# Optimization experiments

Hardware: AMD Instinct MI355X
Metric: run time of the kernel (lower is better)

The kernel has to match this reference:

```python
import jax, jax.numpy as jnp
import numpy as np

EPS = 1e-5

def _layernorm(x, gamma, beta):
    mu = jnp.mean(x, axis=-1, keepdims=True)
    var = jnp.var(x, axis=-1, keepdims=True)
    return (x - mu) * jax.lax.rsqrt(var + EPS) * gamma + beta

def setup_inputs() -> dict:
    key = jax.random.key(0)
    ks = jax.random.split(key, 6)
    bs, t, dim = 4, 2048, 1024
    x = jax.random.normal(ks[0], (bs, t, dim), dtype=jnp.float32)
    # shared LayerNorm params (same module applied twice in forward)
    ln_gamma = jnp.ones((dim,), dtype=jnp.float32)
    ln_beta = jnp.zeros((dim,), dtype=jnp.float32)
    # Linear params, stored as (in, out)
    w1 = jax.random.normal(ks[1], (dim, 2 * dim), dtype=jnp.float32) / np.sqrt(dim)
    b1 = jax.random.normal(ks[2], (2 * dim,), dtype=jnp.float32) * 0.01
    w2 = jax.random.normal(ks[3], (2 * dim, dim), dtype=jnp.float32) / np.sqrt(2 * dim)
    b2 = jax.random.normal(ks[4], (dim,), dtype=jnp.float32) * 0.01
    return {"x": x, "ln_gamma": ln_gamma, "ln_beta": ln_beta,
            "w1": w1, "b1": b1, "w2": w2, "b2": b2}

def reference(x, ln_gamma, ln_beta, w1, b1, w2, b2):
    # x: [bs, t, f]
    y = _layernorm(x, ln_gamma, ln_beta)
    y = jax.nn.gelu(jnp.einsum('btf,fh->bth', y, w1) + b1, approximate=False)
    y = jnp.einsum('bth,hf->btf', y, w2) + b2
    # attention-like quadratic mix (no softmax): (x @ x^T) @ y
    scores = jnp.einsum('btf,bsf->bts', x, x)          # [bs, t, t]
    y = jnp.einsum('bts,bsf->btf', scores, y)
    y = x + y
    y = _layernorm(y, ln_gamma, ln_beta)
    return y
```

## Files before the change

### kernel.cpp

```cpp
#include <hip/hip_runtime.h>
#include <hip/hip_fp16.h>

typedef _Float16 f16;
typedef _Float16 f16x8 __attribute__((ext_vector_type(8)));
typedef _Float16 f16x4 __attribute__((ext_vector_type(4)));
typedef float f32x4 __attribute__((ext_vector_type(4)));

#define LN_EPS 1e-5f

__device__ __forceinline__ float erf_fast(float x) {
    const float ax = __builtin_fabsf(x);
    const float t = 1.0f / (1.0f + 0.3275911f * ax);
    const float y = t * (0.254829592f +
                    t * (-0.284496736f +
                    t * (1.421413741f +
                    t * (-1.453152027f +
                    t * 1.061405429f))));
    const float r = 1.0f - y * __expf(-ax * ax);
    return __builtin_copysignf(r, x);
}

__device__ __forceinline__ float gelu_exact(float v) {
    return 0.5f * v * (1.0f + erf_fast(v * 0.70710678118654752440f));
}

__device__ __forceinline__ void gload_lds16(const f16* g, f16* l) {
    __builtin_amdgcn_global_load_lds(
        (const __attribute__((address_space(1))) unsigned int*)(g),
        (__attribute__((address_space(3))) unsigned int*)(l),
        16, 0, 0);
}

__global__ __launch_bounds__(256)
void ln_cast_kernel(const float* __restrict__ x,
                    const float* __restrict__ gamma,
                    const float* __restrict__ beta,
                    f16* __restrict__ y_h,
                    f16* __restrict__ x_h) {
    const int row = blockIdx.x;
    const int t = threadIdx.x;
    const size_t base = (size_t)row * 1024;
    float4 v = ((const float4*)(x + base))[t];
    float s  = v.x + v.y + v.z + v.w;
    float s2 = v.x*v.x + v.y*v.y + v.z*v.z + v.w*v.w;
    #pragma unroll
    for (int off = 32; off > 0; off >>= 1) {
        s  += __shfl_down(s, off, 64);
        s2 += __shfl_down(s2, off, 64);
    }
    __shared__ float ls[4], ls2[4];
    const int wid = t >> 6;
    if ((t & 63) == 0) { ls[wid] = s; ls2[wid] = s2; }
    __syncthreads();
    if (t == 0) {
        ls[0]  = ls[0] + ls[1] + ls[2] + ls[3];
        ls2[0] = ls2[0] + ls2[1] + ls2[2] + ls2[3];
    }
    __syncthreads();
    const float mu   = ls[0] * (1.0f / 1024.0f);
    const float var  = ls2[0] * (1.0f / 1024.0f) - mu * mu;
    const float rstd = rsqrtf(var + LN_EPS);
    const float4 g  = ((const float4*)gamma)[t];
    const float4 bt = ((const float4*)beta)[t];
    f16x4 yo, xo;
    yo[0] = (f16)((v.x - mu) * rstd * g.x + bt.x);
    yo[1] = (f16)((v.y - mu) * rstd * g.y + bt.y);
    yo[2] = (f16)((v.z - mu) * rstd * g.z + bt.z);
    yo[3] = (f16)((v.w - mu) * rstd * g.w + bt.w);
    xo[0] = (f16)v.x; xo[1] = (f16)v.y; xo[2] = (f16)v.z; xo[3] = (f16)v.w;
    *(f16x4*)(y_h + base + t * 4) = yo;
    *(f16x4*)(x_h + base + t * 4) = xo;
}

__global__ __launch_bounds__(256)
void ln_final_kernel(const f16* __restrict__ pre,
                     const float* __restrict__ gamma,
                     const float* __restrict__ beta,
                     float* __restrict__ out) {
    const int row = blockIdx.x;
    const int t = threadIdx.x;
    const size_t base = (size_t)row * 1024;
    const f16x4 vh = *(const f16x4*)(pre + base + t * 4);
    float4 v;
    v.x = (float)vh[0]; v.y = (float)vh[1]; v.z = (float)vh[2]; v.w = (float)vh[3];
    float s  = v.x + v.y + v.z + v.w;
    float s2 = v.x*v.x + v.y*v.y + v.z*v.z + v.w*v.w;
    #pragma unroll
    for (int off = 32; off > 0; off >>= 1) {
        s  += __shfl_down(s, off, 64);
        s2 += __shfl_down(s2, off, 64);
    }
    __shared__ float ls[4], ls2[4];
    const int wid = t >> 6;
    if ((t & 63) == 0) { ls[wid] = s; ls2[wid] = s2; }
    __syncthreads();
    if (t == 0) {
        ls[0]  = ls[0] + ls[1] + ls[2] + ls[3];
        ls2[0] = ls2[0] + ls2[1] + ls2[2] + ls2[3];
    }
    __syncthreads();
    const float mu   = ls[0] * (1.0f / 1024.0f);
    const float var  = ls2[0] * (1.0f / 1024.0f) - mu * mu;
    const float rstd = rsqrtf(var + LN_EPS);
    const float4 g  = ((const float4*)gamma)[t];
    const float4 bt = ((const float4*)beta)[t];
    float4 o;
    o.x = (v.x - mu) * rstd * g.x + bt.x;
    o.y = (v.y - mu) * rstd * g.y + bt.y;
    o.z = (v.z - mu) * rstd * g.z + bt.z;
    o.w = (v.w - mu) * rstd * g.w + bt.w;
    ((float4*)(out + base))[t] = o;
}

__global__ __launch_bounds__(256)
void transpose_cast_kernel(const float* __restrict__ src,
                           f16* __restrict__ dst, int R, int C) {
    __shared__ float tile[32][33];
    const int c0 = blockIdx.x * 32, r0 = blockIdx.y * 32;
    const int tx = threadIdx.x & 31, ty = threadIdx.x >> 5;
    #pragma unroll
    for (int i = 0; i < 4; ++i) {
        const int r = ty + i * 8;
        tile[r][tx] = src[(size_t)(r0 + r) * C + c0 + tx];
    }
    __syncthreads();
    #pragma unroll
    for (int i = 0; i < 4; ++i) {
        const int r = ty + i * 8;
        dst[(size_t)(c0 + r) * R + r0 + tx] = (f16)tile[tx][r];
    }
}

__global__ __launch_bounds__(256)
void transpose_f16_kernel(const f16* __restrict__ src,
                          f16* __restrict__ dst, int R, int C) {
    __shared__ f16 tile[32][33];
    const size_t zb = (size_t)blockIdx.z * R * C;
    src += zb; dst += zb;
    const int c0 = blockIdx.x * 32, r0 = blockIdx.y * 32;
    const int tx = threadIdx.x & 31, ty = threadIdx.x >> 5;
    #pragma unroll
    for (int i = 0; i < 4; ++i) {
        const int r = ty + i * 8;
        tile[r][tx] = src[(size_t)(r0 + r) * C + c0 + tx];
    }
    __syncthreads();
    #pragma unroll
    for (int i = 0; i < 4; ++i) {
        const int r = ty + i * 8;
        dst[(size_t)(c0 + r) * R + r0 + tx] = tile[tx][r];
    }
}

template <int EPI>
__global__ __launch_bounds__(512, 2)
void gemm256x128_nt_kernel(const f16* __restrict__ A, const f16* __restrict__ Bt,
                           const float* __restrict__ bias,
                           const float* __restrict__ xadd,
                           f16* __restrict__ outH,
                           int M, int N, int K,
                           long long batchA, long long batchB, long long batchC) {
    __shared__ __attribute__((aligned(16))) f16 sA[3][256 * 64];
    __shared__ __attribute__((aligned(16))) f16 sB[3][128 * 64];

    const int z = blockIdx.z;
    A  += (size_t)z * batchA;
    Bt += (size_t)z * batchB;

    const int m0 = blockIdx.x * 256;
    const int n0 = blockIdx.y * 128;
    const int t = threadIdx.x;
    const int l = t & 63;
    const int wid = t >> 6;
    const int wr = wid >> 1;
    const int wc = wid & 1;
    const int rl = l & 15;
    const int g  = l >> 4;
    const int nk = K >> 6;

    const int rowS = t >> 3;
    const int kbS  = ((t & 7) ^ (rowS & 7)) * 8;
    const f16* pA = A  + (size_t)(m0 + rowS) * K + kbS;
    const f16* pB = Bt + (size_t)(n0 + rowS) * K + kbS;
    const int ldsS = wid * 512;

    const int rA = wr * 64 + rl;
    const int rB = wc * 64 + rl;
    const int swk0 = ((g)     ^ (rl & 7)) * 8;
    const int swk1 = ((4 + g) ^ (rl & 7)) * 8;

    f32x4 acc[4][4] = {};

    auto mf = [&](f32x4 c, f16x8 af, f16x8 bf) {
        if constexpr (EPI != 1)
            return __builtin_amdgcn_mfma_f32_16x16x32_f16(bf, af, c, 0, 0, 0);
        else
            return __builtin_amdgcn_mfma_f32_16x16x32_f16(af, bf, c, 0, 0, 0);
    };

    auto stgA = [&](f16* dst, int u, int kc) {
        gload_lds16(pA + (size_t)u * 64 * K + kc * 64, dst + u * 4096 + ldsS);
    };
    auto stgB = [&](f16* dst, int u, int kc) {
        gload_lds16(pB + (size_t)u * 64 * K + kc * 64, dst + u * 4096 + ldsS);
    };

    const int t1 = (nk > 1) ? 1 : 0;
    #pragma unroll
    for (int u = 0; u < 4; ++u) stgA(sA[0], u, 0);
    #pragma unroll
    for (int u = 0; u < 2; ++u) stgB(sB[0], u, 0);
    #pragma unroll
    for (int u = 0; u < 4; ++u) stgA(sA[1], u, t1);
    #pragma unroll
    for (int u = 0; u < 2; ++u) stgB(sB[1], u, t1);

    f16 *curA = sA[0], *nxtA = sA[1], *farA = sA[2];
    f16 *curB = sB[0], *nxtB = sB[1], *farB = sB[2];

    f16x8 a[4][2], b[4][2];

    for (int kt = 0; kt < nk; ++kt) {
        asm volatile("s_waitcnt vmcnt(6)" ::: "memory");
        __builtin_amdgcn_s_barrier();

        const int kt2 = (kt + 2 < nk) ? kt + 2 : nk - 1;

        #pragma unroll
        for (int fm = 0; fm < 2; ++fm) {
            a[fm][0] = *(const f16x8*)(curA + (rA + fm * 16) * 64 + swk0);
            a[fm][1] = *(const f16x8*)(curA + (rA + fm * 16) * 64 + swk1);
        }
        #pragma unroll
        for (int fn = 0; fn < 2; ++fn) {
            b[fn][0] = *(const f16x8*)(curB + (rB + fn * 16) * 64 + swk0);
            b[fn][1] = *(const f16x8*)(curB + (rB + fn * 16) * 64 + swk1);
        }
        stgA(farA, 0, kt2);
        stgA(farA, 1, kt2);
        asm volatile("s_waitcnt lgkmcnt(0)" ::: "memory");
        __builtin_amdgcn_sched_barrier(0);
        __builtin_amdgcn_s_setprio(1);
        #pragma unroll
        for (int fm = 0; fm < 2; ++fm)
            #pragma unroll
            for (int fn = 0; fn < 2; ++fn) {
                acc[fm][fn] = mf(acc[fm][fn], a[fm][0], b[fn][0]);
                acc[fm][fn] = mf(acc[fm][fn], a[fm][1], b[fn][1]);
            }
        __builtin_amdgcn_s_setprio(0);

        #pragma unroll
        for (int fn = 2; fn < 4; ++fn) {
            b[fn][0] = *(const f16x8*)(curB + (rB + fn * 16) * 64 + swk0);
            b[fn][1] = *(const f16x8*)(curB + (rB + fn * 16) * 64 + swk1);
        }
        stgA(farA, 2, kt2);
        stgA(farA, 3, kt2);
        asm volatile("s_waitcnt lgkmcnt(0)" ::: "memory");
        __builtin_amdgcn_sched_barrier(0);
        __builtin_amdgcn_s_setprio(1);
        #pragma unroll
        for (int fm = 0; fm < 2; ++fm)
            #pragma unroll
            for (int fn = 2; fn < 4; ++fn) {
                acc[fm][fn] = mf(acc[fm][fn], a[fm][0], b[fn][0]);
                acc[fm][fn] = mf(acc[fm][fn], a[fm][1], b[fn][1]);
            }
        __builtin_amdgcn_s_setprio(0);

        #pragma unroll
        for (int fm = 2; fm < 4; ++fm) {
            a[fm][0] = *(const f16x8*)(curA + (rA + fm * 16) * 64 + swk0);
            a[fm][1] = *(const f16x8*)(curA + (rA + fm * 16) * 64 + swk1);
        }
        stgB(farB, 0, kt2);
        stgB(farB, 1, kt2);
        asm volatile("s_waitcnt lgkmcnt(0)" ::: "memory");
        __builtin_amdgcn_sched_barrier(0);
        __builtin_amdgcn_s_setprio(1);
        #pragma unroll
        for (int fm = 2; fm < 4; ++fm)
            #pragma unroll
            for (int fn = 2; fn < 4; ++fn) {
                acc[fm][fn] = mf(acc[fm][fn], a[fm][0], b[fn][0]);
                acc[fm][fn] = mf(acc[fm][fn], a[fm][1], b[fn][1]);
            }
        __builtin_amdgcn_s_setprio(0);

        __builtin_amdgcn_s_setprio(1);
        #pragma unroll
        for (int fm = 2; fm < 4; ++fm)
            #pragma unroll
            for (int fn = 0; fn < 2; ++fn) {
                acc[fm][fn] = mf(acc[fm][fn], a[fm][0], b[fn][0]);
                acc[fm][fn] = mf(acc[fm][fn], a[fm][1], b[fn][1]);
            }
        __builtin_amdgcn_s_setprio(0);

        f16* tp;
        tp = curA; curA = nxtA; nxtA = farA; farA = tp;
        tp = curB; curB = nxtB; nxtB = farB; farB = tp;
    }

    if (EPI == 1) {
        __syncthreads();
        f16* lds_t = (f16*)sA;
        #pragma unroll
        for (int fm = 0; fm < 4; ++fm) {
            const int rowb = wr * 64 + fm * 16 + g * 4;
            #pragma unroll
            for (int fn = 0; fn < 4; ++fn) {
                const int cl = wc * 64 + fn * 16 + rl;
                const float bv = bias[n0 + cl];
                f16x4 o;
                #pragma unroll
                for (int r = 0; r < 4; ++r) o[r] = (f16)(acc[fm][fn][r] + bv);
                *(f16x4*)&lds_t[cl * 264 + rowb] = o;
            }
        }
        __syncthreads();
        const int lh = l & 31, ch = l >> 5;
        #pragma unroll
        for (int it = 0; it < 8; ++it) {
            const int c = it * 16 + wid * 2 + ch;
            const f16x8 vv = *(const f16x8*)&lds_t[c * 264 + lh * 8];
            const int rowg = m0 + lh * 8;
            const int zz = rowg >> 11, rr = rowg & 2047;
            *(f16x8*)(outH + ((size_t)zz * N + (n0 + c)) * 2048 + rr) = vv;
        }
    } else {
        asm volatile("s_waitcnt vmcnt(0)" ::: "memory");
        const float* xaddz = xadd;
        f16* outHz = outH;
        if (EPI == 3) {
            outHz += (size_t)z * batchC;
            xaddz += (size_t)z * batchC;
        }
        #pragma unroll
        for (int fm = 0; fm < 4; ++fm) {
            const int row = m0 + wr * 64 + fm * 16 + rl;
            #pragma unroll
            for (int fn = 0; fn < 4; ++fn) {
                const int colb = n0 + wc * 64 + fn * 16 + g * 4;
                if (EPI == 0) {
                    const float4 bv = *(const float4*)&bias[colb];
                    f16x4 o;
                    o[0] = (f16)gelu_exact(acc[fm][fn][0] + bv.x);
                    o[1] = (f16)gelu_exact(acc[fm][fn][1] + bv.y);
                    o[2] = (f16)gelu_exact(acc[fm][fn][2] + bv.z);
                    o[3] = (f16)gelu_exact(acc[fm][fn][3] + bv.w);
                    *(f16x4*)(outH + (size_t)row * N + colb) = o;
                } else {
                    const size_t idx = (size_t)row * N + colb;
                    const float4 xa = *(const float4*)&xaddz[idx];
                    f16x4 o;
                    o[0] = (f16)(acc[fm][fn][0] + xa.x);
                    o[1] = (f16)(acc[fm][fn][1] + xa.y);
                    o[2] = (f16)(acc[fm][fn][2] + xa.z);
                    o[3] = (f16)(acc[fm][fn][3] + xa.w);
                    *(f16x4*)(outHz + idx) = o;
                }
            }
        }
    }
}

__global__ __launch_bounds__(256, 3)
void gemm_nt_kernel(const f16* __restrict__ A, const f16* __restrict__ Bt,
                    f16* __restrict__ outH,
                    int M, int N, int K,
                    long long batchA, long long batchB, long long batchC) {
    __shared__ __attribute__((aligned(16))) f16 sA[3][128 * 32];
    __shared__ __attribute__((aligned(16))) f16 sB[3][128 * 32];

    const int z = blockIdx.z;
    A  += (size_t)z * batchA;
    Bt += (size_t)z * batchB;

    const int m0 = blockIdx.x * 128;
    const int n0 = blockIdx.y * 128;
    const int t = threadIdx.x;
    const int l = t & 63;
    const int wid = t >> 6;
    const int wm = (wid >> 1) * 64;
    const int wn = (wid & 1) * 64;

    f32x4 acc[4][4] = {};

    const int rl = l & 15;
    const int nk = K >> 5;

    const int row0 = t >> 2;
    const int kb = ((t & 3) ^ (row0 & 3)) * 8;
    const f16* Ag0 = A  + (size_t)(m0 + row0) * K + kb;
    const f16* Ag1 = A  + (size_t)(m0 + row0 + 64) * K + kb;
    const f16* Bg0 = Bt + (size_t)(n0 + row0) * K + kb;
    const f16* Bg1 = Bt + (size_t)(n0 + row0 + 64) * K + kb;
    const int lo0 = wid * 512;
    const int lo1 = 2048 + wid * 512;

    const int swk = (((l >> 4) ^ (rl & 3))) * 8;

    gload_lds16(Ag0,      sA[0] + lo0);
    gload_lds16(Ag1,      sA[0] + lo1);
    gload_lds16(Bg0,      sB[0] + lo0);
    gload_lds16(Bg1,      sB[0] + lo1);
    gload_lds16(Ag0 + 32, sA[1] + lo0);
    gload_lds16(Ag1 + 32, sA[1] + lo1);
    gload_lds16(Bg0 + 32, sB[1] + lo0);
    gload_lds16(Bg1 + 32, sB[1] + lo1);

    f16 *curA = sA[0], *nxtA = sA[1], *farA = sA[2];
    f16 *curB = sB[0], *nxtB = sB[1], *farB = sB[2];

    for (int kt = 0; kt < nk; ++kt) {
        asm volatile("s_waitcnt vmcnt(4)" ::: "memory");
        __builtin_amdgcn_s_barrier();
        asm volatile("" ::: "memory");

        const int ktn = (kt + 2 < nk) ? kt + 2 : nk - 1;
        const int kof = ktn * 32;
        gload_lds16(Ag0 + kof, farA + lo0);
        gload_lds16(Ag1 + kof, farA + lo1);
        gload_lds16(Bg0 + kof, farB + lo0);
        gload_lds16(Bg1 + kof, farB + lo1);

        f16x8 a[4], b[4];
        #pragma unroll
        for (int f = 0; f < 4; ++f) {
            a[f] = *(const f16x8*)&curA[(wm + f * 16 + rl) * 32 + swk];
            b[f] = *(const f16x8*)&curB[(wn + f * 16 + rl) * 32 + swk];
        }
        #pragma unroll
        for (int fm = 0; fm < 4; ++fm)
            #pragma unroll
            for (int fn = 0; fn < 4; ++fn)
                acc[fm][fn] = __builtin_amdgcn_mfma_f32_16x16x32_f16(
                    b[fn], a[fm], acc[fm][fn], 0, 0, 0);

        f16* tA = curA; curA = nxtA; nxtA = farA; farA = tA;
        f16* tB = curB; curB = nxtB; nxtB = farB; farB = tB;
    }
    asm volatile("s_waitcnt vmcnt(0)" ::: "memory");

    const int rh = l >> 4;
    f16* outHz = outH + (size_t)z * batchC;
    #pragma unroll
    for (int fm = 0; fm < 4; ++fm) {
        const int row = m0 + wm + fm * 16 + rl;
        #pragma unroll
        for (int fn = 0; fn < 4; ++fn) {
            const int colb = n0 + wn + fn * 16 + rh * 4;
            f16x4 o;
            #pragma unroll
            for (int r = 0; r < 4; ++r) o[r] = (f16)acc[fm][fn][r];
            *(f16x4*)(outHz + (size_t)row * N + colb) = o;
        }
    }
}

extern "C" void kernel_launch(void* const* d_in, const int* in_sizes, int n_in,
                              void* d_out, int out_size, void* d_ws, size_t ws_size,
                              hipStream_t stream) {
    const float* x     = (const float*)d_in[0];
    const float* gamma = (const float*)d_in[1];
    const float* beta  = (const float*)d_in[2];
    const float* w1    = (const float*)d_in[3];
    const float* b1    = (const float*)d_in[4];
    const float* w2    = (const float*)d_in[5];
    const float* b2    = (const float*)d_in[6];
    float* out = (float*)d_out;

    const int BS = 4, T = 2048, DIM = 1024, HID = 2048;
    const int M = BS * T;
    const long long MB = 1024 * 1024;

    char* ws = (char*)d_ws;
    f16*   x_h   = (f16*)(ws + 0 * MB);
    f16*   y_h   = (f16*)(ws + 16 * MB);
    f16*   h     = (f16*)(ws + 32 * MB);
    f16*   pre_h = h;
    f16*   y2t   = (f16*)(ws + 64 * MB);
    f16*   x_t   = (f16*)(ws + 80 * MB);
    f16*   G     = (f16*)(ws + 96 * MB);
    f16*   w1t   = (f16*)(ws + 104 * MB);
    f16*   w2t   = (f16*)(ws + 108 * MB);

    ln_cast_kernel<<<M, 256, 0, stream>>>(x, gamma, beta, y_h, x_h);

    transpose_cast_kernel<<<dim3(HID / 32, DIM / 32), 256, 0, stream>>>(w1, w1t, DIM, HID);
    transpose_cast_kernel<<<dim3(DIM / 32, HID / 32), 256, 0, stream>>>(w2, w2t, HID, DIM);

    gemm256x128_nt_kernel<0><<<dim3(M / 256, HID / 128, 1), 512, 0, stream>>>(
        y_h, w1t, b1, nullptr, h, M, HID, DIM, 0, 0, 0);

    gemm256x128_nt_kernel<1><<<dim3(M / 256, DIM / 128, 1), 512, 0, stream>>>(
        h, w2t, b2, nullptr, y2t, M, DIM, HID, 0, 0, 0);

    transpose_f16_kernel<<<dim3(DIM / 32, T / 32, BS), 256, 0, stream>>>(x_h, x_t, T, DIM);

    gemm_nt_kernel<<<dim3(DIM / 128, DIM / 128, BS), 256, 0, stream>>>(
        y2t, x_t, G, DIM, DIM, T,
        (long long)DIM * T, (long long)DIM * T, (long long)DIM * DIM);

    gemm256x128_nt_kernel<3><<<dim3(T / 256, DIM / 128, BS), 512, 0, stream>>>(
        x_h, G, nullptr, x, pre_h, T, DIM, DIM,
        (long long)T * DIM, (long long)DIM * DIM, (long long)T * DIM);

    ln_final_kernel<<<M, 256, 0, stream>>>(pre_h, gamma, beta, out);
}
```

Baseline: 197.7 us.

## Split-K the Gram GEMM on the 256x128 kernel and merge weight transposes

The batched G = y2t·x_tᵀ GEMM (K=2048) moves from the 128x128 kernel onto the larger 256x128 MFMA kernel, which gains leading-dimension parameters. K is split in two halves across an extra grid z-dimension, and a small gsum kernel adds the two fp16 partials. The two weight transpose-casts are folded into one launch. The aim is more blocks in flight for the small 1024x1024 output tiles and fewer launches, at the cost of an extra partial-sum pass and a second fp16 rounding of G.

```diff
diff --git a/kernel.cpp b/kernel.cpp
--- a/kernel.cpp
+++ b/kernel.cpp
@@ -113,10 +113,18 @@
 }
 
 __global__ __launch_bounds__(256)
-void transpose_cast_kernel(const float* __restrict__ src,
-                           f16* __restrict__ dst, int R, int C) {
+void wt_transpose_kernel(const float* __restrict__ w1, const float* __restrict__ w2,
+                         f16* __restrict__ w1t, f16* __restrict__ w2t) {
     __shared__ float tile[32][33];
-    const int c0 = blockIdx.x * 32, r0 = blockIdx.y * 32;
+    int bid = blockIdx.x;
+    const float* src; f16* dst; int R, C, cx, ry;
+    if (bid < 2048) {
+        src = w1; dst = w1t; R = 1024; C = 2048; cx = bid & 63; ry = bid >> 6;
+    } else {
+        bid -= 2048;
+        src = w2; dst = w2t; R = 2048; C = 1024; cx = bid & 31; ry = bid >> 5;
+    }
+    const int c0 = cx * 32, r0 = ry * 32;
     const int tx = threadIdx.x & 31, ty = threadIdx.x >> 5;
     #pragma unroll
     for (int i = 0; i < 4; ++i) {
@@ -152,20 +160,38 @@
     }
 }
 
+__global__ __launch_bounds__(256)
+void gsum_kernel(f16* __restrict__ g) {
+    const size_t per = (size_t)1024 * 1024;
+    f16* a = g + (size_t)blockIdx.y * 2 * per
+               + (size_t)blockIdx.x * 2048 + (size_t)threadIdx.x * 8;
+    const f16* b = a + per;
+    f16x8 va = *(f16x8*)a;
+    const f16x8 vb = *(const f16x8*)b;
+    #pragma unroll
+    for (int i = 0; i < 8; ++i) va[i] = (f16)((float)va[i] + (float)vb[i]);
+    *(f16x8*)a = va;
+}
+
 template <int EPI>
 __global__ __launch_bounds__(512, 2)
 void gemm256x128_nt_kernel(const f16* __restrict__ A, const f16* __restrict__ Bt,
                            const float* __restrict__ bias,
                            const float* __restrict__ xadd,
                            f16* __restrict__ outH,
-                           int M, int N, int K,
+                           int M, int N, int K, int ldA, int ldB,
                            long long batchA, long long batchB, long long batchC) {
     __shared__ __attribute__((aligned(16))) f16 sA[3][256 * 64];
     __shared__ __attribute__((aligned(16))) f16 sB[3][128 * 64];
 
     const int z = blockIdx.z;
-    A  += (size_t)z * batchA;
-    Bt += (size_t)z * batchB;
+    if (EPI == 2) {
+        A  += (size_t)(z >> 1) * batchA + (size_t)(z & 1) * 1024;
+        Bt += (size_t)(z >> 1) * batchB + (size_t)(z & 1) * 1024;
+    } else {
+        A  += (size_t)z * batchA;
+        Bt += (size_t)z * batchB;
+    }
 
     const int m0 = blockIdx.x * 256;
     const int n0 = blockIdx.y * 128;
@@ -180,8 +206,8 @@
 
     const int rowS = t >> 3;
     const int kbS  = ((t & 7) ^ (rowS & 7)) * 8;
-    const f16* pA = A  + (size_t)(m0 + rowS) * K + kbS;
-    const f16* pB = Bt + (size_t)(n0 + rowS) * K + kbS;
+    const f16* pA = A  + (size_t)(m0 + rowS) * ldA + kbS;
+    const f16* pB = Bt + (size_t)(n0 + rowS) * ldB + kbS;
     const int ldsS = wid * 512;
 
     const int rA = wr * 64 + rl;
@@ -199,10 +225,10 @@
     };
 
     auto stgA = [&](f16* dst, int u, int kc) {
-        gload_lds16(pA + (size_t)u * 64 * K + kc * 64, dst + u * 4096 + ldsS);
+        gload_lds16(pA + (size_t)u * 64 * ldA + kc * 64, dst + u * 4096 + ldsS);
     };
     auto stgB = [&](f16* dst, int u, int kc) {
-        gload_lds16(pB + (size_t)u * 64 * K + kc * 64, dst + u * 4096 + ldsS);
+        gload_lds16(pB + (size_t)u * 64 * ldB + kc * 64, dst + u * 4096 + ldsS);
     };
 
     const int t1 = (nk > 1) ? 1 : 0;
@@ -333,9 +359,9 @@
         asm volatile("s_waitcnt vmcnt(0)" ::: "memory");
         const float* xaddz = xadd;
         f16* outHz = outH;
-        if (EPI == 3) {
+        if (EPI == 3 || EPI == 2) {
             outHz += (size_t)z * batchC;
-            xaddz += (size_t)z * batchC;
+            if (EPI == 3) xaddz += (size_t)z * batchC;
         }
         #pragma unroll
         for (int fm = 0; fm < 4; ++fm) {
@@ -351,6 +377,11 @@
                     o[2] = (f16)gelu_exact(acc[fm][fn][2] + bv.z);
                     o[3] = (f16)gelu_exact(acc[fm][fn][3] + bv.w);
                     *(f16x4*)(outH + (size_t)row * N + colb) = o;
+                } else if (EPI == 2) {
+                    f16x4 o;
+                    #pragma unroll
+                    for (int r = 0; r < 4; ++r) o[r] = (f16)acc[fm][fn][r];
+                    *(f16x4*)(outHz + (size_t)row * N + colb) = o;
                 } else {
                     const size_t idx = (size_t)row * N + colb;
                     const float4 xa = *(const float4*)&xaddz[idx];
@@ -362,100 +393,6 @@
                     *(f16x4*)(outHz + idx) = o;
                 }
             }
-        }
-    }
-}
-
-__global__ __launch_bounds__(256, 3)
-void gemm_nt_kernel(const f16* __restrict__ A, const f16* __restrict__ Bt,
-                    f16* __restrict__ outH,
-                    int M, int N, int K,
-                    long long batchA, long long batchB, long long batchC) {
-    __shared__ __attribute__((aligned(16))) f16 sA[3][128 * 32];
-    __shared__ __attribute__((aligned(16))) f16 sB[3][128 * 32];
-
-    const int z = blockIdx.z;
-    A  += (size_t)z * batchA;
-    Bt += (size_t)z * batchB;
-
-    const int m0 = blockIdx.x * 128;
-    const int n0 = blockIdx.y * 128;
-    const int t = threadIdx.x;
-    const int l = t & 63;
-    const int wid = t >> 6;
-    const int wm = (wid >> 1) * 64;
-    const int wn = (wid & 1) * 64;
-
-    f32x4 acc[4][4] = {};
-
-    const int rl = l & 15;
-    const int nk = K >> 5;
-
-    const int row0 = t >> 2;
-    const int kb = ((t & 3) ^ (row0 & 3)) * 8;
-    const f16* Ag0 = A  + (size_t)(m0 + row0) * K + kb;
-    const f16* Ag1 = A  + (size_t)(m0 + row0 + 64) * K + kb;
-    const f16* Bg0 = Bt + (size_t)(n0 + row0) * K + kb;
-    const f16* Bg1 = Bt + (size_t)(n0 + row0 + 64) * K + kb;
-    const int lo0 = wid * 512;
-    const int lo1 = 2048 + wid * 512;
-
-    const int swk = (((l >> 4) ^ (rl & 3))) * 8;
-
-    gload_lds16(Ag0,      sA[0] + lo0);
-    gload_lds16(Ag1,      sA[0] + lo1);
-    gload_lds16(Bg0,      sB[0] + lo0);
-    gload_lds16(Bg1,      sB[0] + lo1);
-    gload_lds16(Ag0 + 32, sA[1] + lo0);
-    gload_lds16(Ag1 + 32, sA[1] + lo1);
-    gload_lds16(Bg0 + 32, sB[1] + lo0);
-    gload_lds16(Bg1 + 32, sB[1] + lo1);
-
-    f16 *curA = sA[0], *nxtA = sA[1], *farA = sA[2];
-    f16 *curB = sB[0], *nxtB = sB[1], *farB = sB[2];
-
-    for (int kt = 0; kt < nk; ++kt) {
-        asm volatile("s_waitcnt vmcnt(4)" ::: "memory");
-        __builtin_amdgcn_s_barrier();
-        asm volatile("" ::: "memory");
-
-        const int ktn = (kt + 2 < nk) ? kt + 2 : nk - 1;
-        const int kof = ktn * 32;
-        gload_lds16(Ag0 + kof, farA + lo0);
-        gload_lds16(Ag1 + kof, farA + lo1);
-        gload_lds16(Bg0 + kof, farB + lo0);
-        gload_lds16(Bg1 + kof, farB + lo1);
-
-        f16x8 a[4], b[4];
-        #pragma unroll
-        for (int f = 0; f < 4; ++f) {
-            a[f] = *(const f16x8*)&curA[(wm + f * 16 + rl) * 32 + swk];
-            b[f] = *(const f16x8*)&curB[(wn + f * 16 + rl) * 32 + swk];
-        }
-        #pragma unroll
-        for (int fm = 0; fm < 4; ++fm)
-            #pragma unroll
-            for (int fn = 0; fn < 4; ++fn)
-                acc[fm][fn] = __builtin_amdgcn_mfma_f32_16x16x32_f16(
-                    b[fn], a[fm], acc[fm][fn], 0, 0, 0);
-
-        f16* tA = curA; curA = nxtA; nxtA = farA; farA = tA;
-        f16* tB = curB; curB = nxtB; nxtB = farB; farB = tB;
-    }
-    asm volatile("s_waitcnt vmcnt(0)" ::: "memory");
-
-    const int rh = l >> 4;
-    f16* outHz = outH + (size_t)z * batchC;
-    #pragma unroll
-    for (int fm = 0; fm < 4; ++fm) {
-        const int row = m0 + wm + fm * 16 + rl;
-        #pragma unroll
-        for (int fn = 0; fn < 4; ++fn) {
-            const int colb = n0 + wn + fn * 16 + rh * 4;
-            f16x4 o;
-            #pragma unroll
-            for (int r = 0; r < 4; ++r) o[r] = (f16)acc[fm][fn][r];
-            *(f16x4*)(outHz + (size_t)row * N + colb) = o;
         }
     }
 }
@@ -483,30 +420,31 @@
     f16*   pre_h = h;
     f16*   y2t   = (f16*)(ws + 64 * MB);
     f16*   x_t   = (f16*)(ws + 80 * MB);
-    f16*   G     = (f16*)(ws + 96 * MB);
-    f16*   w1t   = (f16*)(ws + 104 * MB);
-    f16*   w2t   = (f16*)(ws + 108 * MB);
+    f16*   Gpair = (f16*)(ws + 96 * MB);
+    f16*   w1t   = (f16*)(ws + 112 * MB);
+    f16*   w2t   = (f16*)(ws + 116 * MB);
 
     ln_cast_kernel<<<M, 256, 0, stream>>>(x, gamma, beta, y_h, x_h);
 
-    transpose_cast_kernel<<<dim3(HID / 32, DIM / 32), 256, 0, stream>>>(w1, w1t, DIM, HID);
-    transpose_cast_kernel<<<dim3(DIM / 32, HID / 32), 256, 0, stream>>>(w2, w2t, HID, DIM);
+    wt_transpose_kernel<<<4096, 256, 0, stream>>>(w1, w2, w1t, w2t);
 
     gemm256x128_nt_kernel<0><<<dim3(M / 256, HID / 128, 1), 512, 0, stream>>>(
-        y_h, w1t, b1, nullptr, h, M, HID, DIM, 0, 0, 0);
+        y_h, w1t, b1, nullptr, h, M, HID, DIM, DIM, DIM, 0, 0, 0);
 
     gemm256x128_nt_kernel<1><<<dim3(M / 256, DIM / 128, 1), 512, 0, stream>>>(
-        h, w2t, b2, nullptr, y2t, M, DIM, HID, 0, 0, 0);
+        h, w2t, b2, nullptr, y2t, M, DIM, HID, HID, HID, 0, 0, 0);
 
     transpose_f16_kernel<<<dim3(DIM / 32, T / 32, BS), 256, 0, stream>>>(x_h, x_t, T, DIM);
 
-    gemm_nt_kernel<<<dim3(DIM / 128, DIM / 128, BS), 256, 0, stream>>>(
-        y2t, x_t, G, DIM, DIM, T,
+    gemm256x128_nt_kernel<2><<<dim3(DIM / 256, DIM / 128, BS * 2), 512, 0, stream>>>(
+        y2t, x_t, nullptr, nullptr, Gpair, DIM, DIM, T / 2, T, T,
         (long long)DIM * T, (long long)DIM * T, (long long)DIM * DIM);
 
+    gsum_kernel<<<dim3(512, BS), 256, 0, stream>>>(Gpair);
+
     gemm256x128_nt_kernel<3><<<dim3(T / 256, DIM / 128, BS), 512, 0, stream>>>(
-        x_h, G, nullptr, x, pre_h, T, DIM, DIM,
-        (long long)T * DIM, (long long)DIM * DIM, (long long)T * DIM);
+        x_h, Gpair, nullptr, x, pre_h, T, DIM, DIM, DIM, DIM,
+        (long long)T * DIM, (long long)2 * DIM * DIM, (long long)T * DIM);
 
     ln_final_kernel<<<M, 256, 0, stream>>>(pre_h, gamma, beta, out);
 }
```

New measurement: 182.3 us. 1.08x faster.
